# Kernel tuning notes

Hardware: AMD Instinct MI355X
Metric: run time of the kernel (lower is better)

Reference implementation:

```python
import jax, jax.numpy as jnp
import numpy as np

B, DV, DT, H, G, E = 4096, 1024, 1024, 1024, 4096, 8
D = DV + DT  # fused dim = 2048


def setup_inputs() -> dict:
    key = jax.random.key(0)
    ks = jax.random.split(key, 8)
    s = 0.02
    return {
        "vision_cls": jax.random.normal(ks[0], (B, DV), jnp.float32),
        "text_cls": jax.random.normal(ks[1], (B, DT), jnp.float32),
        "W1_imm": jax.random.normal(ks[2], (E, D, H), jnp.float32) * s,
        "b1_imm": jnp.zeros((E, H), jnp.float32),
        "W2_imm": jax.random.normal(ks[3], (E, H, 1), jnp.float32) * s,
        "b2_imm": jnp.zeros((E, 1), jnp.float32),
        "W1_gene": jax.random.normal(ks[4], (E, D, H), jnp.float32) * s,
        "b1_gene": jnp.zeros((E, H), jnp.float32),
        "W2_gene": jax.random.normal(ks[5], (E, H, G), jnp.float32) * s,
        "b2_gene": jnp.zeros((E, G), jnp.float32),
        "organ_idx": jax.random.randint(ks[6], (B,), 0, E, jnp.int32),
    }


def reference(vision_cls, text_cls, W1_imm, b1_imm, W2_imm, b2_imm,
              W1_gene, b1_gene, W2_gene, b2_gene, organ_idx):
    # fused features [B, D]
    fused = jnp.concatenate([vision_cls, text_cls], axis=-1)
    # Dense MoE reference: run every organ head on the full batch, then
    # select each sample's routed output (same math as the per-group
    # gather -> MLP -> scatter in the original; dropout is eval-mode identity).
    h_i = jax.nn.relu(jnp.einsum('bd,edh->ebh', fused, W1_imm) + b1_imm[:, None, :])
    imm_all = jnp.einsum('ebh,eh->eb', h_i, W2_imm[:, :, 0]) + b2_imm[:, :1]  # [E,B]
    h_g = jax.nn.relu(jnp.einsum('bd,edh->ebh', fused, W1_gene) + b1_gene[:, None, :])
    gene_all = jnp.einsum('ebh,ehg->ebg', h_g, W2_gene) + b2_gene[:, None, :]  # [E,B,G]
    bidx = jnp.arange(fused.shape[0])
    immune = imm_all[organ_idx, bidx]      # [B]
    gene = gene_all[organ_idx, bidx]       # [B,G] (uniform gene_dim -> no padding needed)
    return immune, gene, vision_cls, text_cls
```

## Files before the change

kernel.cpp:

```cpp
#include <hip/hip_runtime.h>


#define B_N 4096
#define DV  1024
#define DD  2048
#define HH  1024
#define GG  4096
#define EE  8
#define BM  128
#define MAXRB 40
#define PERM_N (MAXRB * BM)

typedef __bf16 bf16x8 __attribute__((ext_vector_type(8)));
typedef float f32x4 __attribute__((ext_vector_type(4)));
typedef unsigned short u16x8v __attribute__((ext_vector_type(8)));

#define H_CNT 0
#define H_FIL 8
#define H_OFF 16
#define H_NRB 24
#define H_BLK 32

static __device__ __forceinline__ unsigned short f2bf(float f) {
  return __builtin_bit_cast(unsigned short, (__bf16)f);
}
static __device__ __forceinline__ float bf2f(unsigned short s) {
  return __builtin_bit_cast(float, (unsigned)s << 16);
}
static __device__ __forceinline__ void gload16(const void* g, void* l) {
  __builtin_amdgcn_global_load_lds(
      (const __attribute__((address_space(1))) unsigned int*)g,
      (__attribute__((address_space(3))) unsigned int*)l, 16, 0, 0);
}

__global__ __launch_bounds__(1024) void routing(const int* __restrict__ organ,
                                                int* __restrict__ hdr,
                                                int* __restrict__ perm) {
  __shared__ int cnt[EE], fil[EE], off[EE];
  const int tid = threadIdx.x;
  if (tid < EE) { cnt[tid] = 0; fil[tid] = 0; }
  __syncthreads();
#pragma unroll
  for (int i = 0; i < 4; ++i) atomicAdd(&cnt[organ[tid + (i << 10)]], 1);
#pragma unroll
  for (int i = 0; i < 5; ++i) perm[tid + (i << 10)] = -1;
  __syncthreads();
  if (tid == 0) {
    int acc = 0;
    for (int e = 0; e < EE; ++e) {
      off[e] = acc;
      hdr[H_OFF + e] = acc;
      hdr[H_CNT + e] = cnt[e];
      int nb = (cnt[e] + BM - 1) >> 7;
      int rb0 = acc >> 7;
      for (int i = 0; i < nb; ++i) hdr[H_BLK + rb0 + i] = e;
      acc += nb << 7;
    }
    hdr[H_NRB] = acc >> 7;
  }
  __syncthreads();
#pragma unroll
  for (int i = 0; i < 4; ++i) {
    int b = tid + (i << 10);
    int e = organ[b];
    int slot = off[e] + atomicAdd(&fil[e], 1);
    perm[slot] = b;
  }
}

static __device__ __forceinline__ void wcvt_body(
    const float* __restrict__ in, unsigned short* __restrict__ out,
    int K, int N, int bx, unsigned short* ls) {
  const int nn = N >> 6, nk = K >> 6;
  const int e = bx / (nk * nn);
  int rem = bx - e * nk * nn;
  const int K0 = (rem / nn) << 6, N0 = (rem % nn) << 6;
  const size_t ein = (size_t)e * K * N;
  const int tid = threadIdx.x;
  const int kr = tid >> 4, n0 = (tid & 15) << 2;
#pragma unroll
  for (int p = 0; p < 4; ++p) {
    int k = (p << 4) + kr;
    float4 f = *(const float4*)&in[ein + (size_t)(K0 + k) * N + N0 + n0];
    ls[(n0 + 0) * 72 + k] = f2bf(f.x);
    ls[(n0 + 1) * 72 + k] = f2bf(f.y);
    ls[(n0 + 2) * 72 + k] = f2bf(f.z);
    ls[(n0 + 3) * 72 + k] = f2bf(f.w);
  }
  __syncthreads();
  const int n = tid >> 2, kc = (tid & 3) << 4;
  u16x8v a = *(const u16x8v*)&ls[n * 72 + kc];
  u16x8v b = *(const u16x8v*)&ls[n * 72 + kc + 8];
  size_t o = (size_t)e * N * K + (size_t)(N0 + n) * K + K0 + kc;
  *(u16x8v*)&out[o] = a;
  *(u16x8v*)&out[o + 8] = b;
}

static __device__ __forceinline__ void abuild_body(
    int bx, const float* __restrict__ vis, const float* __restrict__ txt,
    const int* __restrict__ hdr, const int* __restrict__ perm,
    unsigned short* __restrict__ Abuf) {
  const int nr = hdr[H_NRB] << 7;
  const int tid = threadIdx.x;
  const int c = tid << 3;
  const float* srcbase = (c < DV) ? vis : txt;
  const int cc = (c < DV) ? c : c - DV;
#pragma unroll
  for (int p = 0; p < 4; ++p) {
    int r = (bx << 2) + p;
    if (r >= nr) return;
    int smp = perm[r];
    u16x8v v;
    if (smp >= 0) {
      const float* src = srcbase + (size_t)smp * 1024 + cc;
      float4 a = *(const float4*)src, b = *(const float4*)(src + 4);
      v[0] = f2bf(a.x); v[1] = f2bf(a.y); v[2] = f2bf(a.z); v[3] = f2bf(a.w);
      v[4] = f2bf(b.x); v[5] = f2bf(b.y); v[6] = f2bf(b.z); v[7] = f2bf(b.w);
    } else {
#pragma unroll
      for (int i = 0; i < 8; ++i) v[i] = 0;
    }
    *(u16x8v*)&Abuf[(size_t)r * DD + c] = v;
  }
}

static __device__ __forceinline__ void copy_body(
    int bx, const float4* __restrict__ v, const float4* __restrict__ t,
    float4* __restrict__ ov, float4* __restrict__ ot) {
  const int n4 = B_N * DV / 4;
  for (int i = bx * 256 + (int)threadIdx.x; i < n4; i += 1024 * 256) {
    ov[i] = v[i];
    ot[i] = t[i];
  }
}

template <int KDIM>
static __device__ __forceinline__ void gemm_bb(
    const unsigned short* __restrict__ Aseg,
    const unsigned short* __restrict__ Bseg,
    unsigned short* smem, f32x4 (&acc)[4][4]) {
  const int tid = threadIdx.x;
  const int lane = tid & 63;
  const int wr = ((tid >> 6) >> 1) << 6, wc = ((tid >> 6) & 1) << 6;
  const int lr = lane & 15;
  const int arow = tid >> 2;
  const int kq = (((tid & 3) ^ ((arow >> 1) & 3)) << 3);
  const int wbase = (tid & 192) << 3;
  const int bn = tid & 127;
  const int bc0 = (tid >> 7) << 1;
  const int bs = (bn >> 1) & 3;
  const int bslot0 = ((bc0 ^ bs) << 3);
  const int bslot1 = (((bc0 + 1) ^ bs) << 3);
  constexpr int NT = KDIM / 32;

  u16x8v bvE[2], bvO[2];

  auto issueA = [&](int ab, int k0) {
    unsigned short* d = smem + ab * 4096 + wbase;
    gload16(Aseg + (size_t)arow * KDIM + k0 + kq, d);
    gload16(Aseg + (size_t)(64 + arow) * KDIM + k0 + kq, d + 2048);
  };
  auto issueB = [&](u16x8v (&bv)[2], int k0) {
    const unsigned short* p = Bseg + (size_t)bn * KDIM + k0 + (bc0 << 3);
    bv[0] = *(const u16x8v*)p;
    bv[1] = *(const u16x8v*)(p + 8);
  };
  auto writeB = [&](int bb, u16x8v (&bv)[2]) {
    unsigned short* row = smem + 12288 + bb * 4096 + (bn << 5);
    *(u16x8v*)(row + bslot0) = bv[0];
    *(u16x8v*)(row + bslot1) = bv[1];
  };
  auto compute = [&](int ab, int bb) {
    bf16x8 af[4], bfr[4];
#pragma unroll
    for (int m = 0; m < 4; ++m) {
      const int r = wr + m * 16 + lr;
      const int cs = ((lane >> 4) ^ ((r >> 1) & 3)) << 3;
      af[m] = *(const bf16x8*)&smem[ab * 4096 + r * 32 + cs];
    }
#pragma unroll
    for (int n = 0; n < 4; ++n) {
      const int fr = wc + n * 16 + lr;
      const int cs = ((lane >> 4) ^ ((fr >> 1) & 3)) << 3;
      bfr[n] = *(const bf16x8*)&smem[12288 + bb * 4096 + fr * 32 + cs];
    }
#pragma unroll
    for (int m = 0; m < 4; ++m)
#pragma unroll
      for (int n = 0; n < 4; ++n)
        acc[m][n] = __builtin_amdgcn_mfma_f32_16x16x32_bf16(af[m], bfr[n], acc[m][n], 0, 0, 0);
  };

  issueA(0, 0);
  __builtin_amdgcn_sched_barrier(0);
  issueB(bvE, 0);
  writeB(0, bvE);
  issueA(1, 32);
  __builtin_amdgcn_sched_barrier(0);
  issueB(bvO, 32);
  asm volatile("s_waitcnt lgkmcnt(0)" ::: "memory");
  __builtin_amdgcn_s_barrier();
  __builtin_amdgcn_sched_barrier(0);

  auto phase = [&](int t, int abI, int abC, u16x8v (&bvIss)[2],
                   u16x8v (&bvWr)[2], int bbW, int bbC) {
    if (t + 2 < NT) issueA(abI, (t + 2) << 5);
    __builtin_amdgcn_sched_barrier(0);
    if (t + 2 < NT) issueB(bvIss, (t + 2) << 5);
    __builtin_amdgcn_sched_barrier(0);
    compute(abC, bbC);
    if (t + 1 < NT) writeB(bbW, bvWr);
    asm volatile("s_waitcnt lgkmcnt(0)" ::: "memory");
    __builtin_amdgcn_s_barrier();
    __builtin_amdgcn_sched_barrier(0);
  };

  int abI = 2, abC = 0;
  for (int t = 0; t < NT; t += 2) {
    phase(t, abI, abC, bvE, bvO, 1, 0);
    abI = (abI == 2) ? 0 : abI + 1;
    abC = (abC == 2) ? 0 : abC + 1;
    phase(t + 1, abI, abC, bvO, bvE, 0, 1);
    abI = (abI == 2) ? 0 : abI + 1;
    abC = (abC == 2) ? 0 : abC + 1;
  }
}

#define G_CVT1 (EE * (DD >> 6) * (HH >> 6))
#define G_AB   (PERM_N / 4)
__global__ __launch_bounds__(256) void k_prep(
    const float* __restrict__ W1i, const float* __restrict__ W1g,
    unsigned short* __restrict__ W1i_t, unsigned short* __restrict__ W1g_t,
    const float* __restrict__ vis, const float* __restrict__ txt,
    const int* __restrict__ hdr, const int* __restrict__ perm,
    unsigned short* __restrict__ Abuf) {
  __shared__ __align__(16) unsigned short sm[64 * 72];
  int bx = blockIdx.x;
  if (bx < G_CVT1) { wcvt_body(W1i, W1i_t, DD, HH, bx, sm); return; }
  bx -= G_CVT1;
  if (bx < G_CVT1) { wcvt_body(W1g, W1g_t, DD, HH, bx, sm); return; }
  bx -= G_CVT1;
  abuild_body(bx, vis, txt, hdr, perm, Abuf);
}

#define G_G1   (MAXRB * 16)
#define G_CVT2 (EE * (HH >> 6) * (GG >> 6))
#define G_COPY 1024
__global__ __launch_bounds__(256) void k_main1(
    const unsigned short* __restrict__ Abuf,
    const unsigned short* __restrict__ W1i_t, const unsigned short* __restrict__ W1g_t,
    const float* __restrict__ b1i, const float* __restrict__ b1g,
    const int* __restrict__ hdr, unsigned short* __restrict__ H1,
    unsigned short* __restrict__ H2, const float* __restrict__ W2g,
    unsigned short* __restrict__ W2g_t, const float4* __restrict__ vis4,
    const float4* __restrict__ txt4, float4* __restrict__ ov,
    float4* __restrict__ ot) {
  __shared__ __align__(16) unsigned short smem[20480];
  int bx = blockIdx.x;
  if (bx >= G_G1) {
    bx -= G_G1;
    if (bx < G_CVT2) { wcvt_body(W2g, W2g_t, HH, GG, bx, smem); return; }
    copy_body(bx - G_CVT2, vis4, txt4, ov, ot);
    return;
  }
  const int id = (bx & 7) * (G_G1 >> 3) + (bx >> 3);
  const int rb = id % MAXRB;
  if (rb >= hdr[H_NRB]) return;
  const int sub = id / MAXRB, head = sub >> 3, cb = (sub & 7) << 7;
  const int e = hdr[H_BLK + rb];
  const unsigned short* Wt = (head ? W1g_t : W1i_t) + (size_t)e * HH * DD + (size_t)cb * DD;
  const float* bias = (head ? b1g : b1i) + e * HH;
  unsigned short* Hout = head ? H2 : H1;
  const int tid = threadIdx.x;
  const int lane = tid & 63, wave = tid >> 6;
  const int wr = (wave >> 1) << 6, wc = (wave & 1) << 6;
  const int lr = lane & 15;

  f32x4 acc[4][4];
#pragma unroll
  for (int m = 0; m < 4; ++m)
#pragma unroll
    for (int n = 0; n < 4; ++n) acc[m][n] = (f32x4){0.f, 0.f, 0.f, 0.f};

  gemm_bb<DD>(Abuf + (size_t)rb * BM * DD, Wt, smem, acc);
  __syncthreads();

  const int r0l = wr + ((lane >> 4) << 2);
#pragma unroll
  for (int n = 0; n < 4; ++n) {
    const int col = wc + n * 16 + lr;
    const float bv = bias[cb + col];
#pragma unroll
    for (int m = 0; m < 4; ++m)
#pragma unroll
      for (int v = 0; v < 4; ++v) {
        int row = r0l + m * 16 + v;
        float x = acc[m][n][v] + bv;
        x = x > 0.f ? x : 0.f;
        smem[((row << 7) + col) ^ ((row & 7) << 3)] = f2bf(x);
      }
  }
  __syncthreads();
#pragma unroll
  for (int c = 0; c < 8; ++c) {
    int q = c * 256 + tid;
    int row = q >> 4, ch = q & 15;
    int off = ((row << 7) + (ch << 3)) ^ ((row & 7) << 3);
    u16x8v val = *(const u16x8v*)&smem[off];
    *(u16x8v*)&Hout[(size_t)(rb * BM + row) * HH + cb + (ch << 3)] = val;
  }
}

static __device__ __forceinline__ void immune_body(
    int bx, const int* __restrict__ hdr, const int* __restrict__ perm,
    const unsigned short* __restrict__ H1, const float* __restrict__ W2,
    const float* __restrict__ b2, float* __restrict__ out) {
  const int nrb = hdr[H_NRB];
  const int r = bx * 4 + (threadIdx.x >> 6);
  if (r >= nrb * BM) return;
  const int b = perm[r];
  if (b < 0) return;
  const int e = hdr[H_BLK + (r >> 7)];
  const int lane = threadIdx.x & 63;
  const unsigned short* h = H1 + (size_t)r * HH + lane * 16;
  const float* w = W2 + (size_t)e * HH + lane * 16;
  float s = 0.f;
#pragma unroll
  for (int i = 0; i < 16; ++i) s += bf2f(h[i]) * w[i];
#pragma unroll
  for (int off = 32; off >= 1; off >>= 1) s += __shfl_xor(s, off, 64);
  if (lane == 0) out[b] = s + b2[e];
}

#define G_G2 (MAXRB * 32)
__global__ __launch_bounds__(256) void k_main2(
    const unsigned short* __restrict__ H2buf,
    const unsigned short* __restrict__ W2g_t, const float* __restrict__ b2g,
    const int* __restrict__ hdr, const int* __restrict__ perm,
    float* __restrict__ outg, const unsigned short* __restrict__ H1,
    const float* __restrict__ W2i, const float* __restrict__ b2i,
    float* __restrict__ outi) {
  __shared__ __align__(16) unsigned short smem[20480];
  int bx = blockIdx.x;
  if (bx >= G_G2) {
    immune_body(bx - G_G2, hdr, perm, H1, W2i, b2i, outi);
    return;
  }
  const int id = (bx & 7) * (G_G2 >> 3) + (bx >> 3);
  const int rb = id % MAXRB;
  if (rb >= hdr[H_NRB]) return;
  const int cb = (id / MAXRB) << 7;
  const int e = hdr[H_BLK + rb];
  const unsigned short* Wt = W2g_t + (size_t)e * GG * HH + (size_t)cb * HH;
  const int tid = threadIdx.x;
  const int lane = tid & 63, wave = tid >> 6;
  const int wr = (wave >> 1) << 6, wc = (wave & 1) << 6;
  const int lr = lane & 15;

  f32x4 acc[4][4];
#pragma unroll
  for (int m = 0; m < 4; ++m)
#pragma unroll
    for (int n = 0; n < 4; ++n) acc[m][n] = (f32x4){0.f, 0.f, 0.f, 0.f};

  gemm_bb<HH>(H2buf + (size_t)rb * BM * HH, Wt, smem, acc);
  __syncthreads();

  const int r0l = wr + ((lane >> 4) << 2);
#pragma unroll
  for (int n = 0; n < 4; ++n) {
    const int col = wc + n * 16 + lr;
    const float bv = b2g[e * GG + cb + col];
#pragma unroll
    for (int m = 0; m < 4; ++m)
#pragma unroll
      for (int v = 0; v < 4; ++v) {
        int row = r0l + m * 16 + v;
        smem[((row << 7) + col) ^ ((row & 7) << 3)] = f2bf(acc[m][n][v] + bv);
      }
  }
  __syncthreads();
#pragma unroll
  for (int c = 0; c < 8; ++c) {
    int q = c * 256 + tid;
    int row = q >> 4, ch = q & 15;
    int sm = perm[rb * BM + row];
    if (sm < 0) continue;
    int off = ((row << 7) + (ch << 3)) ^ ((row & 7) << 3);
    u16x8v val = *(const u16x8v*)&smem[off];
    float4 f0, f1;
    f0.x = bf2f(val[0]); f0.y = bf2f(val[1]); f0.z = bf2f(val[2]); f0.w = bf2f(val[3]);
    f1.x = bf2f(val[4]); f1.y = bf2f(val[5]); f1.z = bf2f(val[6]); f1.w = bf2f(val[7]);
    float* dst = outg + (size_t)sm * GG + cb + (ch << 3);
    *(float4*)dst = f0;
    *(float4*)(dst + 4) = f1;
  }
}

extern "C" void kernel_launch(void* const* d_in, const int* in_sizes, int n_in,
                              void* d_out, int out_size, void* d_ws, size_t ws_size,
                              hipStream_t stream) {
  (void)in_sizes; (void)n_in; (void)out_size; (void)ws_size;
  const float* vis = (const float*)d_in[0];
  const float* txt = (const float*)d_in[1];
  const float* W1i = (const float*)d_in[2];
  const float* b1i = (const float*)d_in[3];
  const float* W2i = (const float*)d_in[4];
  const float* b2i = (const float*)d_in[5];
  const float* W1g = (const float*)d_in[6];
  const float* b1g = (const float*)d_in[7];
  const float* W2g = (const float*)d_in[8];
  const float* b2g = (const float*)d_in[9];
  const int* organ = (const int*)d_in[10];

  float* out_imm = (float*)d_out;
  float* out_gene = out_imm + B_N;
  float* out_vis = out_gene + (size_t)B_N * GG;
  float* out_txt = out_vis + (size_t)B_N * DV;

  int* hdr = (int*)d_ws;
  int* perm = hdr + 128;

  const size_t OFF_ABUF = 32768;
  const size_t OFF_H1 = OFF_ABUF + (size_t)PERM_N * DD * 2;
  const size_t OFF_H2 = OFF_H1 + (size_t)PERM_N * HH * 2;
  const size_t OFF_W1I = OFF_H2 + (size_t)PERM_N * HH * 2;
  const size_t OFF_W1G = OFF_W1I + (size_t)EE * HH * DD * 2;
  const size_t OFF_W2G = OFF_W1G + (size_t)EE * HH * DD * 2;
  unsigned short* Abuf = (unsigned short*)((char*)d_ws + OFF_ABUF);
  unsigned short* H1 = (unsigned short*)((char*)d_ws + OFF_H1);
  unsigned short* H2 = (unsigned short*)((char*)d_ws + OFF_H2);
  unsigned short* W1i_t = (unsigned short*)((char*)d_ws + OFF_W1I);
  unsigned short* W1g_t = (unsigned short*)((char*)d_ws + OFF_W1G);
  unsigned short* W2g_t = (unsigned short*)((char*)d_ws + OFF_W2G);

  routing<<<1, 1024, 0, stream>>>(organ, hdr, perm);
  k_prep<<<G_CVT1 * 2 + G_AB, 256, 0, stream>>>(W1i, W1g, W1i_t, W1g_t, vis,
                                                txt, hdr, perm, Abuf);
  k_main1<<<G_G1 + G_CVT2 + G_COPY, 256, 0, stream>>>(
      Abuf, W1i_t, W1g_t, b1i, b1g, hdr, H1, H2, W2g, W2g_t,
      (const float4*)vis, (const float4*)txt, (float4*)out_vis,
      (float4*)out_txt);
  k_main2<<<G_G2 + PERM_N / 4, 256, 0, stream>>>(H2, W2g_t, b2g, hdr, perm,
                                                 out_gene, H1, W2i, b2i,
                                                 out_imm);
}
```

Baseline: 252.7 us.

## Fuse immune second layer into first GEMM epilogue via atomic row reductions

The immune head's H-to-1 projection now runs inside the first-layer GEMM epilogue. Each tile reduces relu(acc+b1)*W2 across lanes with shuffles and atomically adds per-row partials into the output, which the routing kernel pre-initialises with the bias. This removes the H1 intermediate buffer write and read and the separate immune pass in the second kernel. The vis/text copy blocks move from the first main kernel to the second to rebalance work. Float atomics make the immune output order-nondeterministic.

```diff
diff --git a/kernel.cpp b/kernel.cpp
--- a/kernel.cpp
+++ b/kernel.cpp
@@ -35,13 +35,20 @@
 
 __global__ __launch_bounds__(1024) void routing(const int* __restrict__ organ,
                                                 int* __restrict__ hdr,
-                                                int* __restrict__ perm) {
+                                                int* __restrict__ perm,
+                                                const float* __restrict__ b2i,
+                                                float* __restrict__ out_imm) {
   __shared__ int cnt[EE], fil[EE], off[EE];
   const int tid = threadIdx.x;
   if (tid < EE) { cnt[tid] = 0; fil[tid] = 0; }
   __syncthreads();
 #pragma unroll
-  for (int i = 0; i < 4; ++i) atomicAdd(&cnt[organ[tid + (i << 10)]], 1);
+  for (int i = 0; i < 4; ++i) {
+    int b = tid + (i << 10);
+    int e = organ[b];
+    atomicAdd(&cnt[e], 1);
+    out_imm[b] = b2i[e];
+  }
 #pragma unroll
   for (int i = 0; i < 5; ++i) perm[tid + (i << 10)] = -1;
   __syncthreads();
@@ -245,24 +252,17 @@
 
 #define G_G1   (MAXRB * 16)
 #define G_CVT2 (EE * (HH >> 6) * (GG >> 6))
-#define G_COPY 1024
 __global__ __launch_bounds__(256) void k_main1(
     const unsigned short* __restrict__ Abuf,
     const unsigned short* __restrict__ W1i_t, const unsigned short* __restrict__ W1g_t,
     const float* __restrict__ b1i, const float* __restrict__ b1g,
-    const int* __restrict__ hdr, unsigned short* __restrict__ H1,
-    unsigned short* __restrict__ H2, const float* __restrict__ W2g,
-    unsigned short* __restrict__ W2g_t, const float4* __restrict__ vis4,
-    const float4* __restrict__ txt4, float4* __restrict__ ov,
-    float4* __restrict__ ot) {
+    const int* __restrict__ hdr, const int* __restrict__ perm,
+    unsigned short* __restrict__ H2, const float* __restrict__ W2i,
+    float* __restrict__ out_imm, const float* __restrict__ W2g,
+    unsigned short* __restrict__ W2g_t) {
   __shared__ __align__(16) unsigned short smem[20480];
   int bx = blockIdx.x;
-  if (bx >= G_G1) {
-    bx -= G_G1;
-    if (bx < G_CVT2) { wcvt_body(W2g, W2g_t, HH, GG, bx, smem); return; }
-    copy_body(bx - G_CVT2, vis4, txt4, ov, ot);
-    return;
-  }
+  if (bx >= G_G1) { wcvt_body(W2g, W2g_t, HH, GG, bx - G_G1, smem); return; }
   const int id = (bx & 7) * (G_G1 >> 3) + (bx >> 3);
   const int rb = id % MAXRB;
   if (rb >= hdr[H_NRB]) return;
@@ -270,7 +270,6 @@
   const int e = hdr[H_BLK + rb];
   const unsigned short* Wt = (head ? W1g_t : W1i_t) + (size_t)e * HH * DD + (size_t)cb * DD;
   const float* bias = (head ? b1g : b1i) + e * HH;
-  unsigned short* Hout = head ? H2 : H1;
   const int tid = threadIdx.x;
   const int lane = tid & 63, wave = tid >> 6;
   const int wr = (wave >> 1) << 6, wc = (wave & 1) << 6;
@@ -285,67 +284,83 @@
   gemm_bb<DD>(Abuf + (size_t)rb * BM * DD, Wt, smem, acc);
   __syncthreads();
 
-  const int r0l = wr + ((lane >> 4) << 2);
-#pragma unroll
-  for (int n = 0; n < 4; ++n) {
-    const int col = wc + n * 16 + lr;
-    const float bv = bias[cb + col];
+  if (head) {
+    const int r0l = wr + ((lane >> 4) << 2);
+#pragma unroll
+    for (int n = 0; n < 4; ++n) {
+      const int col = wc + n * 16 + lr;
+      const float bv = bias[cb + col];
+#pragma unroll
+      for (int m = 0; m < 4; ++m)
+#pragma unroll
+        for (int v = 0; v < 4; ++v) {
+          int row = r0l + m * 16 + v;
+          float x = acc[m][n][v] + bv;
+          x = x > 0.f ? x : 0.f;
+          smem[((row << 7) + col) ^ ((row & 7) << 3)] = f2bf(x);
+        }
+    }
+    __syncthreads();
+#pragma unroll
+    for (int c = 0; c < 8; ++c) {
+      int q = c * 256 + tid;
+      int row = q >> 4, ch = q & 15;
+      int off = ((row << 7) + (ch << 3)) ^ ((row & 7) << 3);
+      u16x8v val = *(const u16x8v*)&smem[off];
+      *(u16x8v*)&H2[(size_t)(rb * BM + row) * HH + cb + (ch << 3)] = val;
+    }
+  } else {
+    float part[4][4];
 #pragma unroll
     for (int m = 0; m < 4; ++m)
 #pragma unroll
-      for (int v = 0; v < 4; ++v) {
-        int row = r0l + m * 16 + v;
-        float x = acc[m][n][v] + bv;
-        x = x > 0.f ? x : 0.f;
-        smem[((row << 7) + col) ^ ((row & 7) << 3)] = f2bf(x);
-      }
-  }
-  __syncthreads();
-#pragma unroll
-  for (int c = 0; c < 8; ++c) {
-    int q = c * 256 + tid;
-    int row = q >> 4, ch = q & 15;
-    int off = ((row << 7) + (ch << 3)) ^ ((row & 7) << 3);
-    u16x8v val = *(const u16x8v*)&smem[off];
-    *(u16x8v*)&Hout[(size_t)(rb * BM + row) * HH + cb + (ch << 3)] = val;
-  }
-}
-
-static __device__ __forceinline__ void immune_body(
-    int bx, const int* __restrict__ hdr, const int* __restrict__ perm,
-    const unsigned short* __restrict__ H1, const float* __restrict__ W2,
-    const float* __restrict__ b2, float* __restrict__ out) {
-  const int nrb = hdr[H_NRB];
-  const int r = bx * 4 + (threadIdx.x >> 6);
-  if (r >= nrb * BM) return;
-  const int b = perm[r];
-  if (b < 0) return;
-  const int e = hdr[H_BLK + (r >> 7)];
-  const int lane = threadIdx.x & 63;
-  const unsigned short* h = H1 + (size_t)r * HH + lane * 16;
-  const float* w = W2 + (size_t)e * HH + lane * 16;
-  float s = 0.f;
-#pragma unroll
-  for (int i = 0; i < 16; ++i) s += bf2f(h[i]) * w[i];
-#pragma unroll
-  for (int off = 32; off >= 1; off >>= 1) s += __shfl_xor(s, off, 64);
-  if (lane == 0) out[b] = s + b2[e];
-}
-
-#define G_G2 (MAXRB * 32)
+      for (int v = 0; v < 4; ++v) part[m][v] = 0.f;
+#pragma unroll
+    for (int n = 0; n < 4; ++n) {
+      const int col = cb + wc + n * 16 + lr;
+      const float bv = bias[col];
+      const float wv = W2i[e * HH + col];
+#pragma unroll
+      for (int m = 0; m < 4; ++m)
+#pragma unroll
+        for (int v = 0; v < 4; ++v) {
+          float x = acc[m][n][v] + bv;
+          x = x > 0.f ? x : 0.f;
+          part[m][v] += x * wv;
+        }
+    }
+#pragma unroll
+    for (int off = 8; off >= 1; off >>= 1)
+#pragma unroll
+      for (int m = 0; m < 4; ++m)
+#pragma unroll
+        for (int v = 0; v < 4; ++v)
+          part[m][v] += __shfl_xor(part[m][v], off, 64);
+    if (lr == 0) {
+      const int rbase = rb * BM + wr + ((lane >> 4) << 2);
+#pragma unroll
+      for (int m = 0; m < 4; ++m)
+#pragma unroll
+        for (int v = 0; v < 4; ++v) {
+          int b = perm[rbase + m * 16 + v];
+          if (b >= 0) atomicAdd(&out_imm[b], part[m][v]);
+        }
+    }
+  }
+}
+
+#define G_G2   (MAXRB * 32)
+#define G_COPY 1024
 __global__ __launch_bounds__(256) void k_main2(
     const unsigned short* __restrict__ H2buf,
     const unsigned short* __restrict__ W2g_t, const float* __restrict__ b2g,
     const int* __restrict__ hdr, const int* __restrict__ perm,
-    float* __restrict__ outg, const unsigned short* __restrict__ H1,
-    const float* __restrict__ W2i, const float* __restrict__ b2i,
-    float* __restrict__ outi) {
+    float* __restrict__ outg, const float4* __restrict__ vis4,
+    const float4* __restrict__ txt4, float4* __restrict__ ov,
+    float4* __restrict__ ot) {
   __shared__ __align__(16) unsigned short smem[20480];
   int bx = blockIdx.x;
-  if (bx >= G_G2) {
-    immune_body(bx - G_G2, hdr, perm, H1, W2i, b2i, outi);
-    return;
-  }
+  if (bx >= G_G2) { copy_body(bx - G_G2, vis4, txt4, ov, ot); return; }
   const int id = (bx & 7) * (G_G2 >> 3) + (bx >> 3);
   const int rb = id % MAXRB;
   if (rb >= hdr[H_NRB]) return;
@@ -422,26 +437,25 @@
   int* perm = hdr + 128;
 
   const size_t OFF_ABUF = 32768;
-  const size_t OFF_H1 = OFF_ABUF + (size_t)PERM_N * DD * 2;
-  const size_t OFF_H2 = OFF_H1 + (size_t)PERM_N * HH * 2;
+  const size_t OFF_H2 = OFF_ABUF + (size_t)PERM_N * DD * 2;
   const size_t OFF_W1I = OFF_H2 + (size_t)PERM_N * HH * 2;
   const size_t OFF_W1G = OFF_W1I + (size_t)EE * HH * DD * 2;
   const size_t OFF_W2G = OFF_W1G + (size_t)EE * HH * DD * 2;
   unsigned short* Abuf = (unsigned short*)((char*)d_ws + OFF_ABUF);
-  unsigned short* H1 = (unsigned short*)((char*)d_ws + OFF_H1);
   unsigned short* H2 = (unsigned short*)((char*)d_ws + OFF_H2);
   unsigned short* W1i_t = (unsigned short*)((char*)d_ws + OFF_W1I);
   unsigned short* W1g_t = (unsigned short*)((char*)d_ws + OFF_W1G);
   unsigned short* W2g_t = (unsigned short*)((char*)d_ws + OFF_W2G);
 
-  routing<<<1, 1024, 0, stream>>>(organ, hdr, perm);
+  routing<<<1, 1024, 0, stream>>>(organ, hdr, perm, b2i, out_imm);
   k_prep<<<G_CVT1 * 2 + G_AB, 256, 0, stream>>>(W1i, W1g, W1i_t, W1g_t, vis,
                                                 txt, hdr, perm, Abuf);
-  k_main1<<<G_G1 + G_CVT2 + G_COPY, 256, 0, stream>>>(
-      Abuf, W1i_t, W1g_t, b1i, b1g, hdr, H1, H2, W2g, W2g_t,
-      (const float4*)vis, (const float4*)txt, (float4*)out_vis,
-      (float4*)out_txt);
-  k_main2<<<G_G2 + PERM_N / 4, 256, 0, stream>>>(H2, W2g_t, b2g, hdr, perm,
-                                                 out_gene, H1, W2i, b2i,
-                                                 out_imm);
-}
+  k_main1<<<G_G1 + G_CVT2, 256, 0, stream>>>(Abuf, W1i_t, W1g_t, b1i, b1g, hdr,
+                                             perm, H2, W2i, out_imm, W2g,
+                                             W2g_t);
+  k_main2<<<G_G2 + G_COPY, 256, 0, stream>>>(H2, W2g_t, b2g, hdr, perm,
+                                             out_gene, (const float4*)vis,
+                                             (const float4*)txt,
+                                             (float4*)out_vis,
+                                             (float4*)out_txt);
+}
```

Result: slower. 261.6 us (+3.5%).
